# Kernel optimization log

Measured on AMD Instinct MI355X. Metric: run time of the kernel, lower is better.

The kernel has to match this reference:

```python
import jax, jax.numpy as jnp
import numpy as np

B, IN_DIM, UNITS, NUM_K, NUM_S = 4096, 128, 256, 64, 256


def setup_inputs() -> dict:
    key = jax.random.key(0)
    ks = jax.random.split(key, 24)
    d = {
        "X": jax.random.normal(ks[0], (B, IN_DIM), jnp.float32),
        "h_prev": jax.random.normal(ks[1], (B, UNITS), jnp.float32),
        "c_prev": jax.random.normal(ks[2], (B, UNITS), jnp.float32),
        "M_prev": jax.random.normal(ks[3], (B, NUM_K, NUM_S), jnp.float32),
        "k_prev": jax.random.normal(ks[4], (B, NUM_S), jnp.float32),
    }
    rows = IN_DIM + UNITS
    s = 0.05
    d["Wf"] = jax.random.normal(ks[5], (rows, UNITS), jnp.float32) * s
    d["Wt"] = jax.random.normal(ks[6], (rows, UNITS), jnp.float32) * s
    d["Wi"] = jax.random.normal(ks[7], (rows, UNITS), jnp.float32) * s
    d["Wo"] = jax.random.normal(ks[8], (rows, UNITS), jnp.float32) * s
    d["bf"] = jnp.zeros((UNITS,), jnp.float32)
    d["bt"] = jnp.zeros((UNITS,), jnp.float32)
    d["bi"] = jnp.zeros((UNITS,), jnp.float32)
    d["bo"] = jnp.zeros((UNITS,), jnp.float32)
    d["Wk"] = jax.random.normal(ks[9], (UNITS, NUM_S), jnp.float32) * s
    d["bk"] = jnp.zeros((NUM_S,), jnp.float32)
    d["Wr"] = jax.random.normal(ks[10], (NUM_S, UNITS), jnp.float32) * s
    d["Wc"] = jax.random.normal(ks[11], (UNITS, UNITS), jnp.float32) * s
    d["Wh"] = jax.random.normal(ks[12], (NUM_S, UNITS), jnp.float32) * s
    d["We"] = jax.random.normal(ks[13], (UNITS, NUM_S), jnp.float32) * s
    d["be"] = jnp.zeros((NUM_S,), jnp.float32)
    d["Wa"] = jax.random.normal(ks[14], (UNITS, NUM_S), jnp.float32) * s
    d["ba"] = jnp.zeros((NUM_S,), jnp.float32)
    return d


def _l2n(x):
    # matches tf.nn.l2_normalize: x / sqrt(max(sum(x^2), eps))
    return x / jnp.sqrt(jnp.maximum(jnp.sum(x * x, axis=-1, keepdims=True), 1e-12))


def reference(X, h_prev, c_prev, M_prev, k_prev,
              Wf, Wt, Wi, Wo, bf, bt, bi, bo,
              Wk, bk, Wr, Wc, Wh, We, be, Wa, ba):
    sig = jax.nn.sigmoid
    xh = jnp.concatenate([X, h_prev], axis=-1)          # (B, in+units)
    i = sig(xh @ Wi + bi)
    f = sig(xh @ Wf + bf)
    o = sig(xh @ Wo + bo)
    t = sig(xh @ Wt + bt)
    c = f * c_prev + i * t                              # (B, units)

    # tf.keras.losses.cosine_similarity returns NEGATIVE cosine similarity
    cos = jnp.einsum('bks,bs->bk', _l2n(M_prev), _l2n(k_prev))
    alpha = jax.nn.softmax(-cos, axis=-1)               # (B, K)
    r = jnp.einsum('bk,bks->bs', alpha, M_prev)         # content read (B, S)

    rc_1 = sig(r @ Wr + c @ Wc)
    h_curr = o * jnp.tanh(c + rc_1 * (r @ Wh))          # (B, units)

    k_curr = jnp.tanh(h_curr @ Wk + bk)                 # (B, S)
    e = sig(h_curr @ We + be)                           # erase  (B, S)
    a = jnp.tanh(h_curr @ Wa + ba)                      # add    (B, S)
    al = alpha[:, :, None]                              # (B, K, 1)
    M_curr = M_prev * (1.0 - al * e[:, None, :]) + al * a[:, None, :]
    return h_curr, c, M_curr, k_curr
```

## Files before the change

kernel.cpp:

```cpp
#include <hip/hip_runtime.h>
#include <math.h>


#define BATCH 4096
#define INDIM 128
#define UNITS 256
#define NUMK  64
#define NUMS  256

typedef unsigned short u16;
typedef __attribute__((ext_vector_type(4))) float  f32x4;
typedef __attribute__((ext_vector_type(8))) short  s16x8;
typedef __attribute__((ext_vector_type(4))) u16    u16x4;
typedef __attribute__((ext_vector_type(8))) u16    u16x8;

__device__ __forceinline__ float sigf(float x) { return 1.0f / (1.0f + expf(-x)); }

__device__ __forceinline__ u16 f2bf(float x) {
    unsigned u = __float_as_uint(x);
    return (u16)((u + 0x7fffu + ((u >> 16) & 1u)) >> 16);
}
__device__ __forceinline__ float bf2f(u16 h) {
    return __uint_as_float(((unsigned)h) << 16);
}
__device__ __forceinline__ void split_bf(float x, u16& hi, u16& lo) {
    hi = f2bf(x);
    lo = f2bf(x - bf2f(hi));
}

__global__ __launch_bounds__(256) void prep_a1(
    const float* __restrict__ X, const float* __restrict__ hp,
    u16* __restrict__ Ahi, u16* __restrict__ Alo)
{
    const int idx = blockIdx.x * 256 + threadIdx.x;
    const int row = idx / 96;
    const int cg  = (idx - row * 96) * 4;
    float4 v;
    if (cg < INDIM) v = *(const float4*)(X + row * INDIM + cg);
    else            v = *(const float4*)(hp + row * UNITS + (cg - INDIM));
    u16x4 h, l;
    u16 th, tl;
    split_bf(v.x, th, tl); h.x = th; l.x = tl;
    split_bf(v.y, th, tl); h.y = th; l.y = tl;
    split_bf(v.z, th, tl); h.z = th; l.z = tl;
    split_bf(v.w, th, tl); h.w = th; l.w = tl;
    *(u16x4*)(Ahi + row * 384 + cg) = h;
    *(u16x4*)(Alo + row * 384 + cg) = l;
}

__global__ __launch_bounds__(256) void pack_w1(
    const float* __restrict__ Wf, const float* __restrict__ Wt,
    const float* __restrict__ Wi, const float* __restrict__ Wo,
    u16* __restrict__ Whi, u16* __restrict__ Wlo)
{
    const int tid = blockIdx.x * 256 + threadIdx.x;
    const int n  = tid / 48;
    const int k0 = (tid - n * 48) * 8;
    const float* src = (n < 256) ? Wf : (n < 512) ? Wt : (n < 768) ? Wi : Wo;
    const int nc = n & 255;
    u16x8 h, l;
    #pragma unroll
    for (int j = 0; j < 8; ++j) {
        float x = src[(k0 + j) * 256 + nc];
        u16 th, tl;
        split_bf(x, th, tl);
        h[j] = th; l[j] = tl;
    }
    *(u16x8*)(Whi + n * 384 + k0) = h;
    *(u16x8*)(Wlo + n * 384 + k0) = l;
}

__global__ __launch_bounds__(256) void pack_w3(
    const float* __restrict__ Wr, const float* __restrict__ Wc,
    const float* __restrict__ Wh,
    u16* __restrict__ Whi, u16* __restrict__ Wlo)
{
    const int tid = blockIdx.x * 256 + threadIdx.x;
    const int n  = tid / 64;
    const int k0 = (tid - n * 64) * 8;
    u16x8 h, l;
    #pragma unroll
    for (int j = 0; j < 8; ++j) {
        const int k = k0 + j;
        float x;
        if (n < 256) x = (k < 256) ? Wr[k * 256 + n] : Wc[(k - 256) * 256 + n];
        else         x = (k < 256) ? Wh[k * 256 + (n - 256)] : 0.0f;
        u16 th, tl;
        split_bf(x, th, tl);
        h[j] = th; l[j] = tl;
    }
    *(u16x8*)(Whi + n * 512 + k0) = h;
    *(u16x8*)(Wlo + n * 512 + k0) = l;
}

__global__ __launch_bounds__(256) void pack_w4(
    const float* __restrict__ Wk, const float* __restrict__ We,
    const float* __restrict__ Wa,
    u16* __restrict__ Whi, u16* __restrict__ Wlo)
{
    const int tid = blockIdx.x * 256 + threadIdx.x;
    const int n  = tid / 32;
    const int k0 = (tid - n * 32) * 8;
    const float* src = (n < 256) ? Wk : (n < 512) ? We : Wa;
    const int nc = n & 255;
    u16x8 h, l;
    #pragma unroll
    for (int j = 0; j < 8; ++j) {
        float x = src[(k0 + j) * 256 + nc];
        u16 th, tl;
        split_bf(x, th, tl);
        h[j] = th; l[j] = tl;
    }
    *(u16x8*)(Whi + n * 256 + k0) = h;
    *(u16x8*)(Wlo + n * 256 + k0) = l;
}

template<int K>
__global__ __launch_bounds__(256) void gemm_bf16x2(
    const u16* __restrict__ Ahi, const u16* __restrict__ Alo,
    const u16* __restrict__ Bhi, const u16* __restrict__ Blo,
    float* __restrict__ C, int N)
{
    const int t = threadIdx.x;
    const int wave = t >> 6, lane = t & 63;
    const int m0 = blockIdx.x * 64 + wave * 16;
    const int n0 = blockIdx.y * 64;
    const int r = lane & 15, g = lane >> 4;

    const u16* pAh = Ahi + (size_t)(m0 + r) * K + g * 8;
    const u16* pAl = Alo + (size_t)(m0 + r) * K + g * 8;
    const u16* pBh = Bhi + (size_t)(n0 + r) * K + g * 8;
    const u16* pBl = Blo + (size_t)(n0 + r) * K + g * 8;

    f32x4 acc[4];
    #pragma unroll
    for (int j = 0; j < 4; ++j) acc[j] = (f32x4){0.f, 0.f, 0.f, 0.f};

    #pragma unroll 2
    for (int k0 = 0; k0 < K; k0 += 32) {
        s16x8 ah = *(const s16x8*)(pAh + k0);
        s16x8 al = *(const s16x8*)(pAl + k0);
        #pragma unroll
        for (int j = 0; j < 4; ++j) {
            s16x8 bh = *(const s16x8*)(pBh + (size_t)j * 16 * K + k0);
            s16x8 bl = *(const s16x8*)(pBl + (size_t)j * 16 * K + k0);
            acc[j] = __builtin_amdgcn_mfma_f32_16x16x32_bf16(ah, bh, acc[j], 0, 0, 0);
            acc[j] = __builtin_amdgcn_mfma_f32_16x16x32_bf16(al, bh, acc[j], 0, 0, 0);
            acc[j] = __builtin_amdgcn_mfma_f32_16x16x32_bf16(ah, bl, acc[j], 0, 0, 0);
        }
    }

    #pragma unroll
    for (int j = 0; j < 4; ++j)
        #pragma unroll
        for (int rr = 0; rr < 4; ++rr)
            C[(size_t)(m0 + g * 4 + rr) * N + (n0 + j * 16 + r)] = acc[j][rr];
}

__global__ __launch_bounds__(256) void e1(
    const float* __restrict__ G1, const float* __restrict__ c_prev,
    const float* __restrict__ bf, const float* __restrict__ bt,
    const float* __restrict__ bi, const float* __restrict__ bo,
    float* __restrict__ c_out, u16* __restrict__ A3hi, u16* __restrict__ A3lo,
    float* __restrict__ o_ws)
{
    const int idx = blockIdx.x * 256 + threadIdx.x;
    const int row = idx >> 6;
    const int c0  = (idx & 63) * 4;
    const float* g = G1 + (size_t)row * 1024 + c0;
    float4 fv = *(const float4*)(g);
    float4 tv = *(const float4*)(g + 256);
    float4 iv = *(const float4*)(g + 512);
    float4 ov = *(const float4*)(g + 768);
    float4 bfv = *(const float4*)(bf + c0), btv = *(const float4*)(bt + c0);
    float4 biv = *(const float4*)(bi + c0), bov = *(const float4*)(bo + c0);
    float4 cp = *(const float4*)(c_prev + (size_t)row * 256 + c0);
    float fa[4] = {fv.x, fv.y, fv.z, fv.w}, ta[4] = {tv.x, tv.y, tv.z, tv.w};
    float ia[4] = {iv.x, iv.y, iv.z, iv.w}, oa[4] = {ov.x, ov.y, ov.z, ov.w};
    float ba_f[4] = {bfv.x, bfv.y, bfv.z, bfv.w}, ba_t[4] = {btv.x, btv.y, btv.z, btv.w};
    float ba_i[4] = {biv.x, biv.y, biv.z, biv.w}, ba_o[4] = {bov.x, bov.y, bov.z, bov.w};
    float cpa[4] = {cp.x, cp.y, cp.z, cp.w};
    float cv[4], oo[4];
    u16x4 chi, clo;
    #pragma unroll
    for (int j = 0; j < 4; ++j) {
        float f = sigf(fa[j] + ba_f[j]);
        float tt = sigf(ta[j] + ba_t[j]);
        float i = sigf(ia[j] + ba_i[j]);
        oo[j] = sigf(oa[j] + ba_o[j]);
        cv[j] = f * cpa[j] + i * tt;
        u16 th, tl;
        split_bf(cv[j], th, tl);
        chi[j] = th; clo[j] = tl;
    }
    *(float4*)(c_out + (size_t)row * 256 + c0) = make_float4(cv[0], cv[1], cv[2], cv[3]);
    *(float4*)(o_ws + (size_t)row * 256 + c0) = make_float4(oo[0], oo[1], oo[2], oo[3]);
    *(u16x4*)(A3hi + (size_t)row * 512 + 256 + c0) = chi;
    *(u16x4*)(A3lo + (size_t)row * 512 + 256 + c0) = clo;
}

__global__ __launch_bounds__(256) void k2_cosr(
    const float* __restrict__ M, const float* __restrict__ k_prev,
    float* __restrict__ alpha_out, u16* __restrict__ A3hi, u16* __restrict__ A3lo)
{
    const int b = blockIdx.x;
    const int t = threadIdx.x;
    const int lane = t & 63;
    const int w = t >> 6;

    __shared__ float sdot[64][8];
    __shared__ float sssq[64][8];
    __shared__ float salpha[64];
    __shared__ float spr[4][256];

    const float4 k4 = *(const float4*)(k_prev + b * NUMS + lane * 4);
    float kss = k4.x * k4.x + k4.y * k4.y + k4.z * k4.z + k4.w * k4.w;
    #pragma unroll
    for (int m = 1; m < 64; m <<= 1) kss += __shfl_xor(kss, m, 64);
    const float knorm = sqrtf(fmaxf(kss, 1e-12f));

    const float* Mb = M + (size_t)b * (NUMK * NUMS);
    f32x4 mreg[16];
    #pragma unroll
    for (int j = 0; j < 16; ++j)
        mreg[j] = __builtin_nontemporal_load((const f32x4*)(Mb + (w * 16 + j) * NUMS + lane * 4));

    #pragma unroll
    for (int j = 0; j < 16; ++j) {
        const f32x4 m4 = mreg[j];
        float dot = m4.x * k4.x + m4.y * k4.y + m4.z * k4.z + m4.w * k4.w;
        float ssq = m4.x * m4.x + m4.y * m4.y + m4.z * m4.z + m4.w * m4.w;
        #pragma unroll
        for (int m = 1; m < 8; m <<= 1) {
            dot += __shfl_xor(dot, m, 64);
            ssq += __shfl_xor(ssq, m, 64);
        }
        if ((lane & 7) == 0) {
            sdot[w * 16 + j][lane >> 3] = dot;
            sssq[w * 16 + j][lane >> 3] = ssq;
        }
    }
    __syncthreads();

    if (t < 64) {
        float dot = 0.f, ssq = 0.f;
        #pragma unroll
        for (int q = 0; q < 8; ++q) { dot += sdot[t][q]; ssq += sssq[t][q]; }
        const float cosv = dot / (sqrtf(fmaxf(ssq, 1e-12f)) * knorm);
        float v = -cosv;
        float vmax = v;
        #pragma unroll
        for (int m = 1; m < 64; m <<= 1) vmax = fmaxf(vmax, __shfl_xor(vmax, m, 64));
        float e = expf(v - vmax);
        float s = e;
        #pragma unroll
        for (int m = 1; m < 64; m <<= 1) s += __shfl_xor(s, m, 64);
        const float al = e / s;
        salpha[t] = al;
        alpha_out[b * NUMK + t] = al;
    }
    __syncthreads();

    float pr0 = 0.f, pr1 = 0.f, pr2 = 0.f, pr3 = 0.f;
    #pragma unroll
    for (int j = 0; j < 16; ++j) {
        const float al = salpha[w * 16 + j];
        pr0 = fmaf(al, mreg[j].x, pr0);
        pr1 = fmaf(al, mreg[j].y, pr1);
        pr2 = fmaf(al, mreg[j].z, pr2);
        pr3 = fmaf(al, mreg[j].w, pr3);
    }
    *(float4*)&spr[w][lane * 4] = make_float4(pr0, pr1, pr2, pr3);
    __syncthreads();
    const float rv = spr[0][t] + spr[1][t] + spr[2][t] + spr[3][t];
    u16 hi, lo;
    split_bf(rv, hi, lo);
    A3hi[(size_t)b * 512 + t] = hi;
    A3lo[(size_t)b * 512 + t] = lo;
}

__global__ __launch_bounds__(256) void e2(
    const float* __restrict__ G3, const float* __restrict__ c,
    const float* __restrict__ o,
    float* __restrict__ h_out, u16* __restrict__ A4hi, u16* __restrict__ A4lo)
{
    const int idx = blockIdx.x * 256 + threadIdx.x;
    const int row = idx >> 6;
    const int c0  = (idx & 63) * 4;
    float4 rc = *(const float4*)(G3 + (size_t)row * 512 + c0);
    float4 rh = *(const float4*)(G3 + (size_t)row * 512 + 256 + c0);
    float4 cv = *(const float4*)(c + (size_t)row * 256 + c0);
    float4 ov = *(const float4*)(o + (size_t)row * 256 + c0);
    float rca[4] = {rc.x, rc.y, rc.z, rc.w}, rha[4] = {rh.x, rh.y, rh.z, rh.w};
    float ca[4] = {cv.x, cv.y, cv.z, cv.w}, oa[4] = {ov.x, ov.y, ov.z, ov.w};
    float hv[4];
    u16x4 hhi, hlo;
    #pragma unroll
    for (int j = 0; j < 4; ++j) {
        hv[j] = oa[j] * tanhf(ca[j] + sigf(rca[j]) * rha[j]);
        u16 th, tl;
        split_bf(hv[j], th, tl);
        hhi[j] = th; hlo[j] = tl;
    }
    *(float4*)(h_out + (size_t)row * 256 + c0) = make_float4(hv[0], hv[1], hv[2], hv[3]);
    *(u16x4*)(A4hi + (size_t)row * 256 + c0) = hhi;
    *(u16x4*)(A4lo + (size_t)row * 256 + c0) = hlo;
}

__global__ __launch_bounds__(256) void e3(
    const float* __restrict__ G4,
    const float* __restrict__ bk, const float* __restrict__ be,
    const float* __restrict__ ba,
    float* __restrict__ k_out, float* __restrict__ e_ws, float* __restrict__ a_ws)
{
    const int idx = blockIdx.x * 256 + threadIdx.x;
    const int row = idx >> 6;
    const int c0  = (idx & 63) * 4;
    const float* g = G4 + (size_t)row * 768 + c0;
    float4 kv = *(const float4*)(g);
    float4 ev = *(const float4*)(g + 256);
    float4 av = *(const float4*)(g + 512);
    float4 bkv = *(const float4*)(bk + c0), bev = *(const float4*)(be + c0);
    float4 bav = *(const float4*)(ba + c0);
    float ka[4] = {kv.x, kv.y, kv.z, kv.w}, ea[4] = {ev.x, ev.y, ev.z, ev.w};
    float aa[4] = {av.x, av.y, av.z, av.w};
    float bka[4] = {bkv.x, bkv.y, bkv.z, bkv.w}, bea[4] = {bev.x, bev.y, bev.z, bev.w};
    float baa[4] = {bav.x, bav.y, bav.z, bav.w};
    float ko[4], eo[4], ao[4];
    #pragma unroll
    for (int j = 0; j < 4; ++j) {
        ko[j] = tanhf(ka[j] + bka[j]);
        eo[j] = sigf (ea[j] + bea[j]);
        ao[j] = tanhf(aa[j] + baa[j]);
    }
    *(float4*)(k_out + (size_t)row * 256 + c0) = make_float4(ko[0], ko[1], ko[2], ko[3]);
    *(float4*)(e_ws  + (size_t)row * 256 + c0) = make_float4(eo[0], eo[1], eo[2], eo[3]);
    *(float4*)(a_ws  + (size_t)row * 256 + c0) = make_float4(ao[0], ao[1], ao[2], ao[3]);
}

__global__ __launch_bounds__(256) void k5_mup(
    const float* __restrict__ M, const float* __restrict__ alpha,
    const float* __restrict__ e, const float* __restrict__ a,
    float* __restrict__ Mout)
{
    const int b = blockIdx.x;
    const int t = threadIdx.x;
    __shared__ float sal[64];
    if (t < 64) sal[t] = alpha[b * NUMK + t];

    const int s4 = (t & 63) * 4;
    const int kr = t >> 6;
    const float4 e4 = *(const float4*)(e + b * NUMS + s4);
    const float4 a4 = *(const float4*)(a + b * NUMS + s4);
    __syncthreads();

    const float* Mb = M + (size_t)b * (NUMK * NUMS);
    float* Ob = Mout + (size_t)b * (NUMK * NUMS);
    #pragma unroll
    for (int j = 0; j < 16; ++j) {
        const int k = j * 4 + kr;
        const float al = sal[k];
        f32x4 m4 = __builtin_nontemporal_load((const f32x4*)(Mb + k * NUMS + s4));
        f32x4 o4;
        o4.x = m4.x * (1.0f - al * e4.x) + al * a4.x;
        o4.y = m4.y * (1.0f - al * e4.y) + al * a4.y;
        o4.z = m4.z * (1.0f - al * e4.z) + al * a4.z;
        o4.w = m4.w * (1.0f - al * e4.w) + al * a4.w;
        __builtin_nontemporal_store(o4, (f32x4*)(Ob + k * NUMS + s4));
    }
}

extern "C" void kernel_launch(void* const* d_in, const int* in_sizes, int n_in,
                              void* d_out, int out_size, void* d_ws, size_t ws_size,
                              hipStream_t stream)
{
    (void)in_sizes; (void)n_in; (void)out_size; (void)ws_size;

    const float* X      = (const float*)d_in[0];
    const float* h_prev = (const float*)d_in[1];
    const float* c_prev = (const float*)d_in[2];
    const float* M_prev = (const float*)d_in[3];
    const float* k_prev = (const float*)d_in[4];
    const float* Wf = (const float*)d_in[5];
    const float* Wt = (const float*)d_in[6];
    const float* Wi = (const float*)d_in[7];
    const float* Wo = (const float*)d_in[8];
    const float* bf = (const float*)d_in[9];
    const float* bt = (const float*)d_in[10];
    const float* bi = (const float*)d_in[11];
    const float* bo = (const float*)d_in[12];
    const float* Wk = (const float*)d_in[13];
    const float* bk = (const float*)d_in[14];
    const float* Wr = (const float*)d_in[15];
    const float* Wc = (const float*)d_in[16];
    const float* Wh = (const float*)d_in[17];
    const float* We = (const float*)d_in[18];
    const float* be = (const float*)d_in[19];
    const float* Wa = (const float*)d_in[20];
    const float* ba = (const float*)d_in[21];

    float* out = (float*)d_out;
    float* h_out = out;
    float* c_out = out + 1048576;
    float* M_out = out + 2097152;
    float* k_out = out + 69206016;

    char* w = (char*)d_ws;
    size_t off = 0;
    auto carve = [&](size_t bytes) { void* p = w + off; off += (bytes + 255) & ~(size_t)255; return p; };
    u16* A1hi = (u16*)carve(4096ull * 384 * 2);
    u16* A1lo = (u16*)carve(4096ull * 384 * 2);
    u16* W1hi = (u16*)carve(1024ull * 384 * 2);
    u16* W1lo = (u16*)carve(1024ull * 384 * 2);
    u16* W3hi = (u16*)carve(512ull * 512 * 2);
    u16* W3lo = (u16*)carve(512ull * 512 * 2);
    u16* W4hi = (u16*)carve(768ull * 256 * 2);
    u16* W4lo = (u16*)carve(768ull * 256 * 2);
    u16* A3hi = (u16*)carve(4096ull * 512 * 2);
    u16* A3lo = (u16*)carve(4096ull * 512 * 2);
    u16* A4hi = (u16*)carve(4096ull * 256 * 2);
    u16* A4lo = (u16*)carve(4096ull * 256 * 2);
    float* G1  = (float*)carve(4096ull * 1024 * 4);
    float* G3  = (float*)carve(4096ull * 512 * 4);
    float* G4  = (float*)carve(4096ull * 768 * 4);
    float* o_ws  = (float*)carve(4096ull * 256 * 4);
    float* al_ws = (float*)carve(4096ull * 64 * 4);
    float* e_ws  = (float*)carve(4096ull * 256 * 4);
    float* a_ws  = (float*)carve(4096ull * 256 * 4);

    pack_w1<<<192, 256, 0, stream>>>(Wf, Wt, Wi, Wo, W1hi, W1lo);
    pack_w3<<<128, 256, 0, stream>>>(Wr, Wc, Wh, W3hi, W3lo);
    pack_w4<<<96, 256, 0, stream>>>(Wk, We, Wa, W4hi, W4lo);
    prep_a1<<<1536, 256, 0, stream>>>(X, h_prev, A1hi, A1lo);

    k2_cosr<<<4096, 256, 0, stream>>>(M_prev, k_prev, al_ws, A3hi, A3lo);

    gemm_bf16x2<384><<<dim3(64, 16), 256, 0, stream>>>(A1hi, A1lo, W1hi, W1lo, G1, 1024);
    e1<<<1024, 256, 0, stream>>>(G1, c_prev, bf, bt, bi, bo, c_out, A3hi, A3lo, o_ws);

    gemm_bf16x2<512><<<dim3(64, 8), 256, 0, stream>>>(A3hi, A3lo, W3hi, W3lo, G3, 512);
    e2<<<1024, 256, 0, stream>>>(G3, c_out, o_ws, h_out, A4hi, A4lo);

    gemm_bf16x2<256><<<dim3(64, 12), 256, 0, stream>>>(A4hi, A4lo, W4hi, W4lo, G4, 768);
    e3<<<1024, 256, 0, stream>>>(G4, bk, be, ba, k_out, e_ws, a_ws);

    k5_mup<<<4096, 256, 0, stream>>>(M_prev, al_ws, e_ws, a_ws, M_out);
}
```

Before: 681.3 us.

## Fuse gate epilogues into GEMMs and merge weight packing kernels

Each GEMM now computes all gate columns for a given output column in one block, so the sigmoid/tanh epilogues run directly on the accumulators. This removes the G1/G3/G4 intermediate buffers, their write-back and re-read, and the separate elementwise launches. The three weight-packing kernels are merged into one launch. Nontemporal loads of M are replaced with plain loads so the second pass over M may hit in cache. The epilogue stores become scalar per-lane writes rather than float4 writes, which may reduce store efficiency.

```diff
diff --git a/kernel.cpp b/kernel.cpp
--- a/kernel.cpp
+++ b/kernel.cpp
@@ -48,155 +48,127 @@
     *(u16x4*)(Alo + row * 384 + cg) = l;
 }
 
-__global__ __launch_bounds__(256) void pack_w1(
+__global__ __launch_bounds__(256) void pack_all(
     const float* __restrict__ Wf, const float* __restrict__ Wt,
     const float* __restrict__ Wi, const float* __restrict__ Wo,
-    u16* __restrict__ Whi, u16* __restrict__ Wlo)
-{
-    const int tid = blockIdx.x * 256 + threadIdx.x;
-    const int n  = tid / 48;
-    const int k0 = (tid - n * 48) * 8;
-    const float* src = (n < 256) ? Wf : (n < 512) ? Wt : (n < 768) ? Wi : Wo;
-    const int nc = n & 255;
-    u16x8 h, l;
-    #pragma unroll
-    for (int j = 0; j < 8; ++j) {
-        float x = src[(k0 + j) * 256 + nc];
-        u16 th, tl;
-        split_bf(x, th, tl);
-        h[j] = th; l[j] = tl;
-    }
-    *(u16x8*)(Whi + n * 384 + k0) = h;
-    *(u16x8*)(Wlo + n * 384 + k0) = l;
-}
-
-__global__ __launch_bounds__(256) void pack_w3(
     const float* __restrict__ Wr, const float* __restrict__ Wc,
     const float* __restrict__ Wh,
-    u16* __restrict__ Whi, u16* __restrict__ Wlo)
-{
-    const int tid = blockIdx.x * 256 + threadIdx.x;
-    const int n  = tid / 64;
-    const int k0 = (tid - n * 64) * 8;
-    u16x8 h, l;
-    #pragma unroll
-    for (int j = 0; j < 8; ++j) {
-        const int k = k0 + j;
-        float x;
-        if (n < 256) x = (k < 256) ? Wr[k * 256 + n] : Wc[(k - 256) * 256 + n];
-        else         x = (k < 256) ? Wh[k * 256 + (n - 256)] : 0.0f;
-        u16 th, tl;
-        split_bf(x, th, tl);
-        h[j] = th; l[j] = tl;
-    }
-    *(u16x8*)(Whi + n * 512 + k0) = h;
-    *(u16x8*)(Wlo + n * 512 + k0) = l;
-}
-
-__global__ __launch_bounds__(256) void pack_w4(
     const float* __restrict__ Wk, const float* __restrict__ We,
     const float* __restrict__ Wa,
-    u16* __restrict__ Whi, u16* __restrict__ Wlo)
-{
-    const int tid = blockIdx.x * 256 + threadIdx.x;
-    const int n  = tid / 32;
-    const int k0 = (tid - n * 32) * 8;
-    const float* src = (n < 256) ? Wk : (n < 512) ? We : Wa;
-    const int nc = n & 255;
-    u16x8 h, l;
-    #pragma unroll
-    for (int j = 0; j < 8; ++j) {
-        float x = src[(k0 + j) * 256 + nc];
-        u16 th, tl;
-        split_bf(x, th, tl);
-        h[j] = th; l[j] = tl;
-    }
-    *(u16x8*)(Whi + n * 256 + k0) = h;
-    *(u16x8*)(Wlo + n * 256 + k0) = l;
-}
-
-template<int K>
-__global__ __launch_bounds__(256) void gemm_bf16x2(
+    u16* __restrict__ W1hi, u16* __restrict__ W1lo,
+    u16* __restrict__ W3hi, u16* __restrict__ W3lo,
+    u16* __restrict__ W4hi, u16* __restrict__ W4lo)
+{
+    const int bid = blockIdx.x;
+    if (bid < 192) {
+        const int tid = bid * 256 + threadIdx.x;
+        const int n  = tid / 48;
+        const int k0 = (tid - n * 48) * 8;
+        const float* src = (n < 256) ? Wf : (n < 512) ? Wt : (n < 768) ? Wi : Wo;
+        const int nc = n & 255;
+        u16x8 h, l;
+        #pragma unroll
+        for (int j = 0; j < 8; ++j) {
+            float x = src[(k0 + j) * 256 + nc];
+            u16 th, tl;
+            split_bf(x, th, tl);
+            h[j] = th; l[j] = tl;
+        }
+        *(u16x8*)(W1hi + n * 384 + k0) = h;
+        *(u16x8*)(W1lo + n * 384 + k0) = l;
+    } else if (bid < 320) {
+        const int tid = (bid - 192) * 256 + threadIdx.x;
+        const int n  = tid / 64;
+        const int k0 = (tid - n * 64) * 8;
+        u16x8 h, l;
+        #pragma unroll
+        for (int j = 0; j < 8; ++j) {
+            const int k = k0 + j;
+            float x;
+            if (n < 256) x = (k < 256) ? Wr[k * 256 + n] : Wc[(k - 256) * 256 + n];
+            else         x = (k < 256) ? Wh[k * 256 + (n - 256)] : 0.0f;
+            u16 th, tl;
+            split_bf(x, th, tl);
+            h[j] = th; l[j] = tl;
+        }
+        *(u16x8*)(W3hi + n * 512 + k0) = h;
+        *(u16x8*)(W3lo + n * 512 + k0) = l;
+    } else {
+        const int tid = (bid - 320) * 256 + threadIdx.x;
+        const int n  = tid / 32;
+        const int k0 = (tid - n * 32) * 8;
+        const float* src = (n < 256) ? Wk : (n < 512) ? We : Wa;
+        const int nc = n & 255;
+        u16x8 h, l;
+        #pragma unroll
+        for (int j = 0; j < 8; ++j) {
+            float x = src[(k0 + j) * 256 + nc];
+            u16 th, tl;
+            split_bf(x, th, tl);
+            h[j] = th; l[j] = tl;
+        }
+        *(u16x8*)(W4hi + n * 256 + k0) = h;
+        *(u16x8*)(W4lo + n * 256 + k0) = l;
+    }
+}
+
+__global__ __launch_bounds__(256) void gemm1_e1(
     const u16* __restrict__ Ahi, const u16* __restrict__ Alo,
     const u16* __restrict__ Bhi, const u16* __restrict__ Blo,
-    float* __restrict__ C, int N)
-{
+    const float* __restrict__ c_prev,
+    const float* __restrict__ bf, const float* __restrict__ bt,
+    const float* __restrict__ bi, const float* __restrict__ bo,
+    float* __restrict__ c_out, float* __restrict__ o_ws,
+    u16* __restrict__ A3hi, u16* __restrict__ A3lo)
+{
+    const int K = 384;
     const int t = threadIdx.x;
     const int wave = t >> 6, lane = t & 63;
     const int m0 = blockIdx.x * 64 + wave * 16;
-    const int n0 = blockIdx.y * 64;
+    const int col0 = blockIdx.y * 16;
     const int r = lane & 15, g = lane >> 4;
 
     const u16* pAh = Ahi + (size_t)(m0 + r) * K + g * 8;
     const u16* pAl = Alo + (size_t)(m0 + r) * K + g * 8;
-    const u16* pBh = Bhi + (size_t)(n0 + r) * K + g * 8;
-    const u16* pBl = Blo + (size_t)(n0 + r) * K + g * 8;
+    const u16* pBh = Bhi + (size_t)(col0 + r) * K + g * 8;
+    const u16* pBl = Blo + (size_t)(col0 + r) * K + g * 8;
 
     f32x4 acc[4];
     #pragma unroll
     for (int j = 0; j < 4; ++j) acc[j] = (f32x4){0.f, 0.f, 0.f, 0.f};
 
     #pragma unroll 2
-    for (int k0 = 0; k0 < K; k0 += 32) {
+    for (int k0 = 0; k0 < 384; k0 += 32) {
         s16x8 ah = *(const s16x8*)(pAh + k0);
         s16x8 al = *(const s16x8*)(pAl + k0);
         #pragma unroll
         for (int j = 0; j < 4; ++j) {
-            s16x8 bh = *(const s16x8*)(pBh + (size_t)j * 16 * K + k0);
-            s16x8 bl = *(const s16x8*)(pBl + (size_t)j * 16 * K + k0);
+            s16x8 bh = *(const s16x8*)(pBh + (size_t)j * 256 * K + k0);
+            s16x8 bl = *(const s16x8*)(pBl + (size_t)j * 256 * K + k0);
             acc[j] = __builtin_amdgcn_mfma_f32_16x16x32_bf16(ah, bh, acc[j], 0, 0, 0);
             acc[j] = __builtin_amdgcn_mfma_f32_16x16x32_bf16(al, bh, acc[j], 0, 0, 0);
             acc[j] = __builtin_amdgcn_mfma_f32_16x16x32_bf16(ah, bl, acc[j], 0, 0, 0);
         }
     }
 
-    #pragma unroll
-    for (int j = 0; j < 4; ++j)
-        #pragma unroll
-        for (int rr = 0; rr < 4; ++rr)
-            C[(size_t)(m0 + g * 4 + rr) * N + (n0 + j * 16 + r)] = acc[j][rr];
-}
-
-__global__ __launch_bounds__(256) void e1(
-    const float* __restrict__ G1, const float* __restrict__ c_prev,
-    const float* __restrict__ bf, const float* __restrict__ bt,
-    const float* __restrict__ bi, const float* __restrict__ bo,
-    float* __restrict__ c_out, u16* __restrict__ A3hi, u16* __restrict__ A3lo,
-    float* __restrict__ o_ws)
-{
-    const int idx = blockIdx.x * 256 + threadIdx.x;
-    const int row = idx >> 6;
-    const int c0  = (idx & 63) * 4;
-    const float* g = G1 + (size_t)row * 1024 + c0;
-    float4 fv = *(const float4*)(g);
-    float4 tv = *(const float4*)(g + 256);
-    float4 iv = *(const float4*)(g + 512);
-    float4 ov = *(const float4*)(g + 768);
-    float4 bfv = *(const float4*)(bf + c0), btv = *(const float4*)(bt + c0);
-    float4 biv = *(const float4*)(bi + c0), bov = *(const float4*)(bo + c0);
-    float4 cp = *(const float4*)(c_prev + (size_t)row * 256 + c0);
-    float fa[4] = {fv.x, fv.y, fv.z, fv.w}, ta[4] = {tv.x, tv.y, tv.z, tv.w};
-    float ia[4] = {iv.x, iv.y, iv.z, iv.w}, oa[4] = {ov.x, ov.y, ov.z, ov.w};
-    float ba_f[4] = {bfv.x, bfv.y, bfv.z, bfv.w}, ba_t[4] = {btv.x, btv.y, btv.z, btv.w};
-    float ba_i[4] = {biv.x, biv.y, biv.z, biv.w}, ba_o[4] = {bov.x, bov.y, bov.z, bov.w};
-    float cpa[4] = {cp.x, cp.y, cp.z, cp.w};
-    float cv[4], oo[4];
-    u16x4 chi, clo;
-    #pragma unroll
-    for (int j = 0; j < 4; ++j) {
-        float f = sigf(fa[j] + ba_f[j]);
-        float tt = sigf(ta[j] + ba_t[j]);
-        float i = sigf(ia[j] + ba_i[j]);
-        oo[j] = sigf(oa[j] + ba_o[j]);
-        cv[j] = f * cpa[j] + i * tt;
-        u16 th, tl;
-        split_bf(cv[j], th, tl);
-        chi[j] = th; clo[j] = tl;
-    }
-    *(float4*)(c_out + (size_t)row * 256 + c0) = make_float4(cv[0], cv[1], cv[2], cv[3]);
-    *(float4*)(o_ws + (size_t)row * 256 + c0) = make_float4(oo[0], oo[1], oo[2], oo[3]);
-    *(u16x4*)(A3hi + (size_t)row * 512 + 256 + c0) = chi;
-    *(u16x4*)(A3lo + (size_t)row * 512 + 256 + c0) = clo;
+    const int col = col0 + r;
+    const float bfv = bf[col], btv = bt[col], biv = bi[col], bov = bo[col];
+    #pragma unroll
+    for (int rr = 0; rr < 4; ++rr) {
+        const int row = m0 + g * 4 + rr;
+        const float cp = c_prev[(size_t)row * 256 + col];
+        const float f  = sigf(acc[0][rr] + bfv);
+        const float tt = sigf(acc[1][rr] + btv);
+        const float i  = sigf(acc[2][rr] + biv);
+        const float o  = sigf(acc[3][rr] + bov);
+        const float cv = f * cp + i * tt;
+        c_out[(size_t)row * 256 + col] = cv;
+        o_ws [(size_t)row * 256 + col] = o;
+        u16 hi, lo;
+        split_bf(cv, hi, lo);
+        A3hi[(size_t)row * 512 + 256 + col] = hi;
+        A3lo[(size_t)row * 512 + 256 + col] = lo;
+    }
 }
 
 __global__ __launch_bounds__(256) void k2_cosr(
@@ -223,7 +195,7 @@
     f32x4 mreg[16];
     #pragma unroll
     for (int j = 0; j < 16; ++j)
-        mreg[j] = __builtin_nontemporal_load((const f32x4*)(Mb + (w * 16 + j) * NUMS + lane * 4));
+        mreg[j] = *(const f32x4*)(Mb + (w * 16 + j) * NUMS + lane * 4);
 
     #pragma unroll
     for (int j = 0; j < 16; ++j) {
@@ -279,63 +251,103 @@
     A3lo[(size_t)b * 512 + t] = lo;
 }
 
-__global__ __launch_bounds__(256) void e2(
-    const float* __restrict__ G3, const float* __restrict__ c,
-    const float* __restrict__ o,
+__global__ __launch_bounds__(256) void gemm3_e2(
+    const u16* __restrict__ Ahi, const u16* __restrict__ Alo,
+    const u16* __restrict__ Bhi, const u16* __restrict__ Blo,
+    const float* __restrict__ c, const float* __restrict__ o,
     float* __restrict__ h_out, u16* __restrict__ A4hi, u16* __restrict__ A4lo)
 {
-    const int idx = blockIdx.x * 256 + threadIdx.x;
-    const int row = idx >> 6;
-    const int c0  = (idx & 63) * 4;
-    float4 rc = *(const float4*)(G3 + (size_t)row * 512 + c0);
-    float4 rh = *(const float4*)(G3 + (size_t)row * 512 + 256 + c0);
-    float4 cv = *(const float4*)(c + (size_t)row * 256 + c0);
-    float4 ov = *(const float4*)(o + (size_t)row * 256 + c0);
-    float rca[4] = {rc.x, rc.y, rc.z, rc.w}, rha[4] = {rh.x, rh.y, rh.z, rh.w};
-    float ca[4] = {cv.x, cv.y, cv.z, cv.w}, oa[4] = {ov.x, ov.y, ov.z, ov.w};
-    float hv[4];
-    u16x4 hhi, hlo;
-    #pragma unroll
-    for (int j = 0; j < 4; ++j) {
-        hv[j] = oa[j] * tanhf(ca[j] + sigf(rca[j]) * rha[j]);
-        u16 th, tl;
-        split_bf(hv[j], th, tl);
-        hhi[j] = th; hlo[j] = tl;
-    }
-    *(float4*)(h_out + (size_t)row * 256 + c0) = make_float4(hv[0], hv[1], hv[2], hv[3]);
-    *(u16x4*)(A4hi + (size_t)row * 256 + c0) = hhi;
-    *(u16x4*)(A4lo + (size_t)row * 256 + c0) = hlo;
-}
-
-__global__ __launch_bounds__(256) void e3(
-    const float* __restrict__ G4,
+    const int K = 512;
+    const int t = threadIdx.x;
+    const int wave = t >> 6, lane = t & 63;
+    const int m0 = blockIdx.x * 64 + wave * 16;
+    const int col0 = blockIdx.y * 16;
+    const int r = lane & 15, g = lane >> 4;
+
+    const u16* pAh = Ahi + (size_t)(m0 + r) * K + g * 8;
+    const u16* pAl = Alo + (size_t)(m0 + r) * K + g * 8;
+    const u16* pBh = Bhi + (size_t)(col0 + r) * K + g * 8;
+    const u16* pBl = Blo + (size_t)(col0 + r) * K + g * 8;
+
+    f32x4 acc[2];
+    acc[0] = (f32x4){0.f, 0.f, 0.f, 0.f};
+    acc[1] = (f32x4){0.f, 0.f, 0.f, 0.f};
+
+    #pragma unroll 2
+    for (int k0 = 0; k0 < 512; k0 += 32) {
+        s16x8 ah = *(const s16x8*)(pAh + k0);
+        s16x8 al = *(const s16x8*)(pAl + k0);
+        #pragma unroll
+        for (int j = 0; j < 2; ++j) {
+            s16x8 bh = *(const s16x8*)(pBh + (size_t)j * 256 * K + k0);
+            s16x8 bl = *(const s16x8*)(pBl + (size_t)j * 256 * K + k0);
+            acc[j] = __builtin_amdgcn_mfma_f32_16x16x32_bf16(ah, bh, acc[j], 0, 0, 0);
+            acc[j] = __builtin_amdgcn_mfma_f32_16x16x32_bf16(al, bh, acc[j], 0, 0, 0);
+            acc[j] = __builtin_amdgcn_mfma_f32_16x16x32_bf16(ah, bl, acc[j], 0, 0, 0);
+        }
+    }
+
+    const int col = col0 + r;
+    #pragma unroll
+    for (int rr = 0; rr < 4; ++rr) {
+        const int row = m0 + g * 4 + rr;
+        const float cv = c[(size_t)row * 256 + col];
+        const float ov = o[(size_t)row * 256 + col];
+        const float hv = ov * tanhf(cv + sigf(acc[0][rr]) * acc[1][rr]);
+        h_out[(size_t)row * 256 + col] = hv;
+        u16 hi, lo;
+        split_bf(hv, hi, lo);
+        A4hi[(size_t)row * 256 + col] = hi;
+        A4lo[(size_t)row * 256 + col] = lo;
+    }
+}
+
+__global__ __launch_bounds__(256) void gemm4_e3(
+    const u16* __restrict__ Ahi, const u16* __restrict__ Alo,
+    const u16* __restrict__ Bhi, const u16* __restrict__ Blo,
     const float* __restrict__ bk, const float* __restrict__ be,
     const float* __restrict__ ba,
     float* __restrict__ k_out, float* __restrict__ e_ws, float* __restrict__ a_ws)
 {
-    const int idx = blockIdx.x * 256 + threadIdx.x;
-    const int row = idx >> 6;
-    const int c0  = (idx & 63) * 4;
-    const float* g = G4 + (size_t)row * 768 + c0;
-    float4 kv = *(const float4*)(g);
-    float4 ev = *(const float4*)(g + 256);
-    float4 av = *(const float4*)(g + 512);
-    float4 bkv = *(const float4*)(bk + c0), bev = *(const float4*)(be + c0);
-    float4 bav = *(const float4*)(ba + c0);
-    float ka[4] = {kv.x, kv.y, kv.z, kv.w}, ea[4] = {ev.x, ev.y, ev.z, ev.w};
-    float aa[4] = {av.x, av.y, av.z, av.w};
-    float bka[4] = {bkv.x, bkv.y, bkv.z, bkv.w}, bea[4] = {bev.x, bev.y, bev.z, bev.w};
-    float baa[4] = {bav.x, bav.y, bav.z, bav.w};
-    float ko[4], eo[4], ao[4];
-    #pragma unroll
-    for (int j = 0; j < 4; ++j) {
-        ko[j] = tanhf(ka[j] + bka[j]);
-        eo[j] = sigf (ea[j] + bea[j]);
-        ao[j] = tanhf(aa[j] + baa[j]);
-    }
-    *(float4*)(k_out + (size_t)row * 256 + c0) = make_float4(ko[0], ko[1], ko[2], ko[3]);
-    *(float4*)(e_ws  + (size_t)row * 256 + c0) = make_float4(eo[0], eo[1], eo[2], eo[3]);
-    *(float4*)(a_ws  + (size_t)row * 256 + c0) = make_float4(ao[0], ao[1], ao[2], ao[3]);
+    const int K = 256;
+    const int t = threadIdx.x;
+    const int wave = t >> 6, lane = t & 63;
+    const int m0 = blockIdx.x * 64 + wave * 16;
+    const int col0 = blockIdx.y * 16;
+    const int r = lane & 15, g = lane >> 4;
+
+    const u16* pAh = Ahi + (size_t)(m0 + r) * K + g * 8;
+    const u16* pAl = Alo + (size_t)(m0 + r) * K + g * 8;
+    const u16* pBh = Bhi + (size_t)(col0 + r) * K + g * 8;
+    const u16* pBl = Blo + (size_t)(col0 + r) * K + g * 8;
+
+    f32x4 acc[3];
+    #pragma unroll
+    for (int j = 0; j < 3; ++j) acc[j] = (f32x4){0.f, 0.f, 0.f, 0.f};
+
+    #pragma unroll 2
+    for (int k0 = 0; k0 < 256; k0 += 32) {
+        s16x8 ah = *(const s16x8*)(pAh + k0);
+        s16x8 al = *(const s16x8*)(pAl + k0);
+        #pragma unroll
+        for (int j = 0; j < 3; ++j) {
+            s16x8 bh = *(const s16x8*)(pBh + (size_t)j * 256 * K + k0);
+            s16x8 bl = *(const s16x8*)(pBl + (size_t)j * 256 * K + k0);
+            acc[j] = __builtin_amdgcn_mfma_f32_16x16x32_bf16(ah, bh, acc[j], 0, 0, 0);
+            acc[j] = __builtin_amdgcn_mfma_f32_16x16x32_bf16(al, bh, acc[j], 0, 0, 0);
+            acc[j] = __builtin_amdgcn_mfma_f32_16x16x32_bf16(ah, bl, acc[j], 0, 0, 0);
+        }
+    }
+
+    const int col = col0 + r;
+    const float bkv = bk[col], bev = be[col], bav = ba[col];
+    #pragma unroll
+    for (int rr = 0; rr < 4; ++rr) {
+        const int row = m0 + g * 4 + rr;
+        k_out[(size_t)row * 256 + col] = tanhf(acc[0][rr] + bkv);
+        e_ws [(size_t)row * 256 + col] = sigf (acc[1][rr] + bev);
+        a_ws [(size_t)row * 256 + col] = tanhf(acc[2][rr] + bav);
+    }
 }
 
 __global__ __launch_bounds__(256) void k5_mup(
@@ -360,7 +372,7 @@
     for (int j = 0; j < 16; ++j) {
         const int k = j * 4 + kr;
         const float al = sal[k];
-        f32x4 m4 = __builtin_nontemporal_load((const f32x4*)(Mb + k * NUMS + s4));
+        f32x4 m4 = *(const f32x4*)(Mb + k * NUMS + s4);
         f32x4 o4;
         o4.x = m4.x * (1.0f - al * e4.x) + al * a4.x;
         o4.y = m4.y * (1.0f - al * e4.y) + al * a4.y;
@@ -420,29 +432,26 @@
     u16* A3lo = (u16*)carve(4096ull * 512 * 2);
     u16* A4hi = (u16*)carve(4096ull * 256 * 2);
     u16* A4lo = (u16*)carve(4096ull * 256 * 2);
-    float* G1  = (float*)carve(4096ull * 1024 * 4);
-    float* G3  = (float*)carve(4096ull * 512 * 4);
-    float* G4  = (float*)carve(4096ull * 768 * 4);
     float* o_ws  = (float*)carve(4096ull * 256 * 4);
     float* al_ws = (float*)carve(4096ull * 64 * 4);
     float* e_ws  = (float*)carve(4096ull * 256 * 4);
     float* a_ws  = (float*)carve(4096ull * 256 * 4);
 
-    pack_w1<<<192, 256, 0, stream>>>(Wf, Wt, Wi, Wo, W1hi, W1lo);
-    pack_w3<<<128, 256, 0, stream>>>(Wr, Wc, Wh, W3hi, W3lo);
-    pack_w4<<<96, 256, 0, stream>>>(Wk, We, Wa, W4hi, W4lo);
+    pack_all<<<416, 256, 0, stream>>>(Wf, Wt, Wi, Wo, Wr, Wc, Wh, Wk, We, Wa,
+                                      W1hi, W1lo, W3hi, W3lo, W4hi, W4lo);
     prep_a1<<<1536, 256, 0, stream>>>(X, h_prev, A1hi, A1lo);
 
+    gemm1_e1<<<dim3(64, 16), 256, 0, stream>>>(A1hi, A1lo, W1hi, W1lo, c_prev,
+                                               bf, bt, bi, bo,
+                                               c_out, o_ws, A3hi, A3lo);
+
     k2_cosr<<<4096, 256, 0, stream>>>(M_prev, k_prev, al_ws, A3hi, A3lo);
 
-    gemm_bf16x2<384><<<dim3(64, 16), 256, 0, stream>>>(A1hi, A1lo, W1hi, W1lo, G1, 1024);
-    e1<<<1024, 256, 0, stream>>>(G1, c_prev, bf, bt, bi, bo, c_out, A3hi, A3lo, o_ws);
-
-    gemm_bf16x2<512><<<dim3(64, 8), 256, 0, stream>>>(A3hi, A3lo, W3hi, W3lo, G3, 512);
-    e2<<<1024, 256, 0, stream>>>(G3, c_out, o_ws, h_out, A4hi, A4lo);
-
-    gemm_bf16x2<256><<<dim3(64, 12), 256, 0, stream>>>(A4hi, A4lo, W4hi, W4lo, G4, 768);
-    e3<<<1024, 256, 0, stream>>>(G4, bk, be, ba, k_out, e_ws, a_ws);
+    gemm3_e2<<<dim3(64, 16), 256, 0, stream>>>(A3hi, A3lo, W3hi, W3lo,
+                                               c_out, o_ws, h_out, A4hi, A4lo);
+
+    gemm4_e3<<<dim3(64, 16), 256, 0, stream>>>(A4hi, A4lo, W4hi, W4lo,
+                                               bk, be, ba, k_out, e_ws, a_ws);
 
     k5_mup<<<4096, 256, 0, stream>>>(M_prev, al_ws, e_ws, a_ws, M_out);
 }
```

After: 697.3 us. +2.4%, slower.
